# Kernel optimization log

Hardware: AMD Instinct MI355X
Metric: run time of the kernel (lower is better)

The kernel has to match this reference:

```python
import jax, jax.numpy as jnp
import numpy as np

NUM_HEADS = 8

def setup_inputs() -> dict:
    key = jax.random.key(0)
    ks = jax.random.split(key, 8)
    B, L, S, D = 4, 2048, 2048, 256
    q = jax.random.normal(ks[0], (B, L, D), dtype=jnp.float32)
    k = jax.random.normal(ks[1], (B, S, D), dtype=jnp.float32)
    self_other_mask = jax.random.bernoulli(ks[2], 0.5, (B, L, S))
    mask = jnp.zeros((B, L, S), dtype=jnp.float32)
    # xavier-uniform-like linear weights (torch Linear weight is [out, in])
    lim = float(np.sqrt(6.0 / (D + D)))
    def w(kk):
        return jax.random.uniform(kk, (D, D), dtype=jnp.float32, minval=-lim, maxval=lim)
    return {
        'q': q, 'k': k, 'self_other_mask': self_other_mask, 'mask': mask,
        'Wq_self': w(ks[3]), 'Wq_other': w(ks[4]),
        'Wk_self': w(ks[5]), 'Wk_other': w(ks[6]),
    }


def reference(q, k, self_other_mask, mask, Wq_self, Wq_other, Wk_self, Wk_other):
    B, L, D = q.shape
    S = k.shape[1]
    H = NUM_HEADS
    hd = D // H
    scale = hd ** -0.5  # qk_scaling
    # projections (torch Linear: x @ W.T), scale applied to queries
    q_self = (q @ Wq_self.T) * scale
    q_other = (q @ Wq_other.T) * scale
    k_self = k @ Wk_self.T
    k_other = k @ Wk_other.T
    # split heads: [B, L, H, hd]
    q_self = q_self.reshape(B, L, H, hd)
    q_other = q_other.reshape(B, L, H, hd)
    k_self = k_self.reshape(B, S, H, hd)
    k_other = k_other.reshape(B, S, H, hd)
    # scores: [B, H, L, S]
    att_self = jnp.einsum('blhd,bshd->bhls', q_self, k_self)
    att_other = jnp.einsum('blhd,bshd->bhls', q_other, k_other)
    # blend by self/other mask (broadcast over heads), then additive mask
    som = self_other_mask[:, None, :, :]  # [B,1,L,S]
    attention = jnp.where(som, att_self, att_other) + mask[:, None, :, :]
    return attention
```

## Files before the change

kernel.cpp:

```cpp
#include <hip/hip_runtime.h>
#include <hip/hip_bf16.h>


typedef __attribute__((ext_vector_type(8))) __bf16 bf16x8;
typedef __attribute__((ext_vector_type(4))) float f32x4;
typedef __attribute__((ext_vector_type(4))) int i32x4;

#define MFMA16(a, b, c) __builtin_amdgcn_mfma_f32_16x16x32_bf16((a), (b), (c), 0, 0, 0)

__device__ __forceinline__ void lds_barrier() {
    asm volatile("s_waitcnt lgkmcnt(0)" ::: "memory");
    __builtin_amdgcn_sched_barrier(0);
    __builtin_amdgcn_s_barrier();
}

__device__ __forceinline__ bf16x8 load8_f32_to_bf16(const float* __restrict__ p) {
    float4 f0 = *(const float4*)p;
    float4 f1 = *(const float4*)(p + 4);
    bf16x8 r;
    r[0] = (__bf16)f0.x; r[1] = (__bf16)f0.y; r[2] = (__bf16)f0.z; r[3] = (__bf16)f0.w;
    r[4] = (__bf16)f1.x; r[5] = (__bf16)f1.y; r[6] = (__bf16)f1.z; r[7] = (__bf16)f1.w;
    return r;
}

__global__ __launch_bounds__(256) void proj_kernel(
    const float* __restrict__ qin, const float* __restrict__ kin,
    const float* __restrict__ Wqs, const float* __restrict__ Wqo,
    const float* __restrict__ Wks, const float* __restrict__ Wko,
    __bf16* __restrict__ qout, __bf16* __restrict__ kout)
{
    const bool isK = blockIdx.y >= 64;
    const float* in = isK ? kin : qin;
    const float* Ws = isK ? Wks : Wqs;
    const float* Wo = isK ? Wko : Wqo;
    __bf16* outp    = isK ? kout : qout;
    const float scale = isK ? 1.0f : 0.17677669529663687f;

    const int n0 = blockIdx.x * 64;
    const int m0 = (blockIdx.y & 63) * 128;
    const int tid  = threadIdx.x;
    const int lane = tid & 63;
    const int w    = tid >> 6;
    const int wr = w >> 1, wc = w & 1;
    const int l15 = lane & 15, l4 = lane >> 4;

    f32x4 acc[4][2];
#pragma unroll
    for (int mi = 0; mi < 4; ++mi)
#pragma unroll
        for (int ni = 0; ni < 2; ++ni) acc[mi][ni] = (f32x4){0.f, 0.f, 0.f, 0.f};

    const int arow0 = m0 + wr * 64 + l15;

    const float* wptr[2];
#pragma unroll
    for (int ni = 0; ni < 2; ++ni) {
        int c = n0 + wc * 32 + ni * 16 + l15;
        wptr[ni] = (c < 256) ? (Ws + c * 256) : (Wo + (c - 256) * 256);
    }

#pragma unroll
    for (int ks = 0; ks < 8; ++ks) {
        const int k0 = ks * 32 + l4 * 8;
        bf16x8 a[4], b[2];
#pragma unroll
        for (int mi = 0; mi < 4; ++mi)
            a[mi] = load8_f32_to_bf16(in + (arow0 + mi * 16) * 256 + k0);
#pragma unroll
        for (int ni = 0; ni < 2; ++ni)
            b[ni] = load8_f32_to_bf16(wptr[ni] + k0);
#pragma unroll
        for (int mi = 0; mi < 4; ++mi)
#pragma unroll
            for (int ni = 0; ni < 2; ++ni)
                acc[mi][ni] = MFMA16(a[mi], b[ni], acc[mi][ni]);
    }

#pragma unroll
    for (int mi = 0; mi < 4; ++mi)
#pragma unroll
        for (int ni = 0; ni < 2; ++ni)
#pragma unroll
            for (int j = 0; j < 4; ++j) {
                int row = m0 + wr * 64 + mi * 16 + l4 * 4 + j;
                int col = n0 + wc * 32 + ni * 16 + l15;
                outp[row * 512 + col] = (__bf16)(acc[mi][ni][j] * scale);
            }
}

__global__ __launch_bounds__(256) void attn_kernel(
    const __bf16* __restrict__ qp, const __bf16* __restrict__ kp,
    const int* __restrict__ som, const float* __restrict__ mask,
    float* __restrict__ out)
{
    __shared__ float tile[32][260];

    const int l0 = blockIdx.x * 32;
    const int s0 = blockIdx.y * 256;
    const int b  = blockIdx.z;
    const int tid  = threadIdx.x;
    const int lane = tid & 63;
    const int w    = tid >> 6;
    const int l15 = lane & 15, l4 = lane >> 4;

    const int c_row = l15;
    const int c_col = w * 64 + l4 * 4;

    f32x4 mreg[2][4];
    unsigned int sbits = 0;
#pragma unroll
    for (int i = 0; i < 8; ++i) {
        int r = w * 8 + i;
        f32x4 m = __builtin_nontemporal_load(
            (const f32x4*)(mask + (long)(b * 2048 + l0 + r) * 2048 + s0 + 4 * lane));
        *(f32x4*)&tile[r][4 * lane] = m;
    }
    __syncthreads();
#pragma unroll
    for (int mi = 0; mi < 2; ++mi)
#pragma unroll
        for (int ni = 0; ni < 4; ++ni)
            mreg[mi][ni] = *(const f32x4*)&tile[c_row + mi * 16][c_col + ni * 16];
    __syncthreads();
#pragma unroll
    for (int i = 0; i < 8; ++i) {
        int r = w * 8 + i;
        i32x4 sm = __builtin_nontemporal_load(
            (const i32x4*)(som + (long)(b * 2048 + l0 + r) * 2048 + s0 + 4 * lane));
        *(i32x4*)&tile[r][4 * lane] = sm;
    }
    __syncthreads();
#pragma unroll
    for (int mi = 0; mi < 2; ++mi)
#pragma unroll
        for (int ni = 0; ni < 4; ++ni) {
            i32x4 sm = *(const i32x4*)&tile[c_row + mi * 16][c_col + ni * 16];
            const int t0 = (mi * 4 + ni) * 4;
#pragma unroll
            for (int j = 0; j < 4; ++j)
                sbits |= (sm[j] != 0) ? (1u << (t0 + j)) : 0u;
        }
    __syncthreads();

    const __bf16* qbase = qp + (long)(b * 2048 + l0 + l15) * 512 + l4 * 8;
    const __bf16* kbase = kp + (long)(b * 2048 + s0 + w * 64 + l15) * 512 + l4 * 8;

    for (int h = 0; h < 8; ++h) {
        const int hofs = h * 32;
        bf16x8 qb[2][2], ka[4][2];
#pragma unroll
        for (int mi = 0; mi < 2; ++mi)
#pragma unroll
            for (int p = 0; p < 2; ++p)
                qb[mi][p] = *(const bf16x8*)(qbase + mi * 16 * 512 + p * 256 + hofs);
#pragma unroll
        for (int ni = 0; ni < 4; ++ni)
#pragma unroll
            for (int p = 0; p < 2; ++p)
                ka[ni][p] = *(const bf16x8*)(kbase + ni * 16 * 512 + p * 256 + hofs);

#pragma unroll
        for (int mi = 0; mi < 2; ++mi)
#pragma unroll
            for (int ni = 0; ni < 4; ++ni) {
                f32x4 z = (f32x4){0.f, 0.f, 0.f, 0.f};
                f32x4 as = MFMA16(ka[ni][0], qb[mi][0], z);
                f32x4 ao = MFMA16(ka[ni][1], qb[mi][1], z);
                const int t0 = (mi * 4 + ni) * 4;
                f32x4 v;
#pragma unroll
                for (int j = 0; j < 4; ++j)
                    v[j] = (((sbits >> (t0 + j)) & 1u) ? as[j] : ao[j]) + mreg[mi][ni][j];
                *(f32x4*)&tile[c_row + mi * 16][c_col + ni * 16] = v;
            }

        lds_barrier();

        const long obase = (long)((b * 8 + h) * 2048 + l0) * 2048 + s0;
#pragma unroll
        for (int i = 0; i < 8; ++i) {
            int r = w * 8 + i;
            f32x4 v = *(const f32x4*)&tile[r][4 * lane];
            *(f32x4*)(out + obase + (long)r * 2048 + 4 * lane) = v;
        }

        lds_barrier();
    }
}

extern "C" void kernel_launch(void* const* d_in, const int* in_sizes, int n_in,
                              void* d_out, int out_size, void* d_ws, size_t ws_size,
                              hipStream_t stream) {
    const float* q    = (const float*)d_in[0];
    const float* k    = (const float*)d_in[1];
    const int*   som  = (const int*)d_in[2];
    const float* mask = (const float*)d_in[3];
    const float* Wqs  = (const float*)d_in[4];
    const float* Wqo  = (const float*)d_in[5];
    const float* Wks  = (const float*)d_in[6];
    const float* Wko  = (const float*)d_in[7];
    float* out = (float*)d_out;

    __bf16* qp = (__bf16*)d_ws;
    __bf16* kp = qp + 8192 * 512;

    dim3 pgrid(8, 128, 1), pblk(256, 1, 1);
    hipLaunchKernelGGL(proj_kernel, pgrid, pblk, 0, stream,
                       q, k, Wqs, Wqo, Wks, Wko, qp, kp);

    dim3 agrid(64, 8, 4), ablk(256, 1, 1);
    hipLaunchKernelGGL(attn_kernel, agrid, ablk, 0, stream, qp, kp, som, mask, out);
}
```

Baseline: 209.5 us.

## Assign one head per block and loop over key tiles, packing som bit into mask

Each block now owns a single head and an L tile, keeps its Q fragments in registers, and loops over all S tiles, rather than owning one (L,S) tile and looping over heads. The som flag is packed into the low mantissa bit of the mask value in LDS, so one shared tile and barrier pass replaces two. The aim is better Q reuse and fewer barriers, at the cost of re-reading mask and som once per head. Packing into the mask LSB slightly alters mask values.

```diff
diff --git a/kernel.cpp b/kernel.cpp
--- a/kernel.cpp
+++ b/kernel.cpp
@@ -5,12 +5,12 @@
 typedef __attribute__((ext_vector_type(8))) __bf16 bf16x8;
 typedef __attribute__((ext_vector_type(4))) float f32x4;
 typedef __attribute__((ext_vector_type(4))) int i32x4;
+typedef __attribute__((ext_vector_type(4))) unsigned int u32x4;
 
 #define MFMA16(a, b, c) __builtin_amdgcn_mfma_f32_16x16x32_bf16((a), (b), (c), 0, 0, 0)
 
 __device__ __forceinline__ void lds_barrier() {
     asm volatile("s_waitcnt lgkmcnt(0)" ::: "memory");
-    __builtin_amdgcn_sched_barrier(0);
     __builtin_amdgcn_s_barrier();
 }
 
@@ -88,15 +88,15 @@
             }
 }
 
-__global__ __launch_bounds__(256) void attn_kernel(
+__global__ __launch_bounds__(256, 4) void attn_kernel(
     const __bf16* __restrict__ qp, const __bf16* __restrict__ kp,
     const int* __restrict__ som, const float* __restrict__ mask,
     float* __restrict__ out)
 {
     __shared__ float tile[32][260];
 
-    const int l0 = blockIdx.x * 32;
-    const int s0 = blockIdx.y * 256;
+    const int h  = blockIdx.x;
+    const int l0 = blockIdx.y * 32;
     const int b  = blockIdx.z;
     const int tid  = threadIdx.x;
     const int lane = tid & 63;
@@ -105,59 +105,58 @@
 
     const int c_row = l15;
     const int c_col = w * 64 + l4 * 4;
-
-    f32x4 mreg[2][4];
-    unsigned int sbits = 0;
-#pragma unroll
-    for (int i = 0; i < 8; ++i) {
-        int r = w * 8 + i;
-        f32x4 m = __builtin_nontemporal_load(
-            (const f32x4*)(mask + (long)(b * 2048 + l0 + r) * 2048 + s0 + 4 * lane));
-        *(f32x4*)&tile[r][4 * lane] = m;
-    }
-    __syncthreads();
+    const int hofs  = h * 32;
+
+    bf16x8 qb[2][2];
 #pragma unroll
     for (int mi = 0; mi < 2; ++mi)
 #pragma unroll
+        for (int p = 0; p < 2; ++p)
+            qb[mi][p] = *(const bf16x8*)(qp + (long)(b * 2048 + l0 + l15 + mi * 16) * 512
+                                            + p * 256 + hofs + l4 * 8);
+
+    const __bf16* kbase = kp + (long)(b * 2048 + w * 64 + l15) * 512 + l4 * 8;
+
+    for (int si = 0; si < 8; ++si) {
+        const int s0 = si * 256;
+
+        bf16x8 ka[4][2];
+#pragma unroll
         for (int ni = 0; ni < 4; ++ni)
-            mreg[mi][ni] = *(const f32x4*)&tile[c_row + mi * 16][c_col + ni * 16];
-    __syncthreads();
-#pragma unroll
-    for (int i = 0; i < 8; ++i) {
-        int r = w * 8 + i;
-        i32x4 sm = __builtin_nontemporal_load(
-            (const i32x4*)(som + (long)(b * 2048 + l0 + r) * 2048 + s0 + 4 * lane));
-        *(i32x4*)&tile[r][4 * lane] = sm;
-    }
-    __syncthreads();
-#pragma unroll
-    for (int mi = 0; mi < 2; ++mi)
-#pragma unroll
-        for (int ni = 0; ni < 4; ++ni) {
-            i32x4 sm = *(const i32x4*)&tile[c_row + mi * 16][c_col + ni * 16];
-            const int t0 = (mi * 4 + ni) * 4;
+#pragma unroll
+            for (int p = 0; p < 2; ++p)
+                ka[ni][p] = *(const bf16x8*)(kbase + (long)(s0 + ni * 16) * 512
+                                                   + p * 256 + hofs);
+
+#pragma unroll
+        for (int i = 0; i < 8; ++i) {
+            int r = w * 8 + i;
+            long gidx = (long)(b * 2048 + l0 + r) * 2048 + s0 + 4 * lane;
+            f32x4 m  = *(const f32x4*)(mask + gidx);
+            i32x4 sm = *(const i32x4*)(som + gidx);
+            u32x4 pk;
 #pragma unroll
             for (int j = 0; j < 4; ++j)
-                sbits |= (sm[j] != 0) ? (1u << (t0 + j)) : 0u;
+                pk[j] = (__float_as_uint(m[j]) & ~1u) | (sm[j] != 0 ? 1u : 0u);
+            *(u32x4*)&tile[r][4 * lane] = pk;
         }
-    __syncthreads();
-
-    const __bf16* qbase = qp + (long)(b * 2048 + l0 + l15) * 512 + l4 * 8;
-    const __bf16* kbase = kp + (long)(b * 2048 + s0 + w * 64 + l15) * 512 + l4 * 8;
-
-    for (int h = 0; h < 8; ++h) {
-        const int hofs = h * 32;
-        bf16x8 qb[2][2], ka[4][2];
+        lds_barrier();
+
+        f32x4 mreg[2][4];
+        unsigned int sbits = 0;
 #pragma unroll
         for (int mi = 0; mi < 2; ++mi)
 #pragma unroll
-            for (int p = 0; p < 2; ++p)
-                qb[mi][p] = *(const bf16x8*)(qbase + mi * 16 * 512 + p * 256 + hofs);
-#pragma unroll
-        for (int ni = 0; ni < 4; ++ni)
-#pragma unroll
-            for (int p = 0; p < 2; ++p)
-                ka[ni][p] = *(const bf16x8*)(kbase + ni * 16 * 512 + p * 256 + hofs);
+            for (int ni = 0; ni < 4; ++ni) {
+                u32x4 pk = *(const u32x4*)&tile[c_row + mi * 16][c_col + ni * 16];
+                const int t0 = (mi * 4 + ni) * 4;
+#pragma unroll
+                for (int j = 0; j < 4; ++j) {
+                    sbits |= (pk[j] & 1u) << (t0 + j);
+                    mreg[mi][ni][j] = __uint_as_float(pk[j] & ~1u);
+                }
+            }
+        lds_barrier();
 
 #pragma unroll
         for (int mi = 0; mi < 2; ++mi)
@@ -173,7 +172,6 @@
                     v[j] = (((sbits >> (t0 + j)) & 1u) ? as[j] : ao[j]) + mreg[mi][ni][j];
                 *(f32x4*)&tile[c_row + mi * 16][c_col + ni * 16] = v;
             }
-
         lds_barrier();
 
         const long obase = (long)((b * 8 + h) * 2048 + l0) * 2048 + s0;
@@ -183,7 +181,6 @@
             f32x4 v = *(const f32x4*)&tile[r][4 * lane];
             *(f32x4*)(out + obase + (long)r * 2048 + 4 * lane) = v;
         }
-
         lds_barrier();
     }
 }
@@ -208,6 +205,6 @@
     hipLaunchKernelGGL(proj_kernel, pgrid, pblk, 0, stream,
                        q, k, Wqs, Wqo, Wks, Wko, qp, kp);
 
-    dim3 agrid(64, 8, 4), ablk(256, 1, 1);
+    dim3 agrid(8, 64, 4), ablk(256, 1, 1);
     hipLaunchKernelGGL(attn_kernel, agrid, ablk, 0, stream, qp, kp, som, mask, out);
 }
```

Result: slower. 324.3 us (+54.8%).
